# Optimization experiments

Hardware: AMD Instinct MI355X
Metric: run time of the kernel (lower is better)

## Reference

```python
import jax, jax.numpy as jnp
import numpy as np

N = 8192
F_IN = 690
F_OUT = 690
H = 3
ALPHA = 0.2  # LeakyReLU negative slope
NEG_INF = -9e15


def setup_inputs() -> dict:
    key = jax.random.key(0)
    k1, k2, k3, k4 = jax.random.split(key, 4)
    x = jax.random.normal(k1, (N, F_IN), dtype=jnp.float32)
    adj = jax.random.randint(k2, (N, N), 0, 2, dtype=jnp.int32)
    adj = adj.at[jnp.arange(N), jnp.arange(N)].set(1)  # self-loops, as in eye() init
    # Xavier-ish scaled params, stacked over heads
    W = jax.random.normal(k3, (H, F_IN, F_OUT), dtype=jnp.float32) * 0.05
    a = jax.random.normal(k4, (H, 2 * F_OUT, 1), dtype=jnp.float32) * 0.05
    return {"x": x, "adj": adj, "W": W, "a": a}


def reference(x, adj, W, a):
    # Wh per head: [H, N, F_OUT]
    Wh = jnp.einsum('nf,hfo->hno', x, W)
    # Additive decomposition of concat-based score: e_ij = leakyrelu(a1_i + a2_j)
    a1 = jnp.einsum('hno,ho->hn', Wh, a[:, :F_OUT, 0])  # [H, N]
    a2 = jnp.einsum('hno,ho->hn', Wh, a[:, F_OUT:, 0])  # [H, N]
    e = jax.nn.leaky_relu(a1[:, :, None] + a2[:, None, :], negative_slope=ALPHA)  # [H, N, N]
    e = jnp.where(adj[None, :, :] > 0, e, NEG_INF)
    attn = jax.nn.softmax(e, axis=-1)
    h_prime = jnp.einsum('hnm,hmo->hno', attn, Wh)  # [H, N, F_OUT]
    # GAT(concat=False): mean over heads, then ELU (dropout is identity in eval)
    y = jax.nn.elu(jnp.mean(h_prime, axis=0))  # [N, F_OUT]
    return y
```

## Files before the change

kernel.cpp:

```cpp
#include <hip/hip_runtime.h>
#include <hip/hip_bf16.h>
#include <stdint.h>

#define NN 8192
#define FD 690
#define NH 3
#define KPAD 704
#define OPAD 768
#define USTRIDE 704
#define KS 2
#define LOG2E 1.4426950408889634f

typedef __attribute__((ext_vector_type(8))) short bf16x8;
typedef __attribute__((ext_vector_type(4))) float f32x4;

typedef __attribute__((address_space(1))) const void gas_t;
typedef __attribute__((address_space(3))) void las_t;

__device__ __forceinline__ void async_ld16(const void* g, void* l) {
  __builtin_amdgcn_global_load_lds((gas_t*)g, (las_t*)l, 16, 0, 0);
}

__device__ __forceinline__ float bf2f(unsigned short u) {
  return __uint_as_float(((unsigned int)u) << 16);
}
__device__ __forceinline__ unsigned short f2bf(float f) {
  __hip_bfloat16 h = __float2bfloat16(f);
  return *reinterpret_cast<unsigned short*>(&h);
}
__device__ __forceinline__ float selbit(float e, uint32_t lo, uint32_t hi) {
  uint64_t m = ((uint64_t)hi << 32) | lo;
  float r;
  asm("v_cndmask_b32 %0, 0, %1, %2" : "=v"(r) : "v"(e), "s"(m));
  return r;
}

__global__ __launch_bounds__(256) void k_cast(const float* __restrict__ x,
                                              const float* __restrict__ W,
                                              unsigned short* __restrict__ xb,
                                              unsigned short* __restrict__ wt) {
  int q = blockIdx.x * 256 + threadIdx.x;
  const int XQ = NN * KPAD / 4;
  if (q < XQ) {
    int idx = q * 4;
    int n = idx / KPAD, f = idx - n * KPAD;
    uint2 out;
    if (f + 3 < FD) {
      const float* xp = &x[(size_t)n * FD + f];
      float2 a = *reinterpret_cast<const float2*>(xp);
      float2 b = *reinterpret_cast<const float2*>(xp + 2);
      out.x = (uint32_t)f2bf(a.x) | ((uint32_t)f2bf(a.y) << 16);
      out.y = (uint32_t)f2bf(b.x) | ((uint32_t)f2bf(b.y) << 16);
    } else {
      unsigned short e[4];
#pragma unroll
      for (int t = 0; t < 4; ++t) {
        int ff = f + t;
        e[t] = (ff < FD) ? f2bf(x[(size_t)n * FD + ff]) : 0;
      }
      out.x = (uint32_t)e[0] | ((uint32_t)e[1] << 16);
      out.y = (uint32_t)e[2] | ((uint32_t)e[3] << 16);
    }
    *reinterpret_cast<uint2*>(&xb[idx]) = out;
    return;
  }
  int idx = q - XQ;
  if (idx >= NH * OPAD * KPAD) return;
  int h = idx / (OPAD * KPAD);
  int rem = idx - h * OPAD * KPAD;
  int o = rem / KPAD, f = rem - o * KPAD;
  float v = (o < FD && f < FD) ? W[((size_t)h * FD + f) * FD + o] : 0.f;
  wt[idx] = f2bf(v);
}

__global__ __launch_bounds__(256) void k_pack(const int4* __restrict__ adj4,
                                              uint64_t* __restrict__ bm) {
  int gw = (blockIdx.x * 256 + threadIdx.x) >> 6;
  int lane = threadIdx.x & 63;
  int i = gw >> 5, seg = gw & 31;
  int4 v = adj4[(size_t)i * (NN / 4) + seg * 64 + lane];
  uint32_t nib = (uint32_t)(v.x > 0) | ((uint32_t)(v.y > 0) << 1)
               | ((uint32_t)(v.z > 0) << 2) | ((uint32_t)(v.w > 0) << 3);
  nib |= __shfl_xor(nib, 1) << 4;
  nib |= __shfl_xor(nib, 2) << 8;
  nib |= __shfl_xor(nib, 4) << 16;
  uint32_t hi = __shfl_xor(nib, 8);
  if ((lane & 15) == 0)
    bm[(size_t)i * 128 + seg * 4 + (lane >> 4)] = (uint64_t)nib | ((uint64_t)hi << 32);
}

__global__ __launch_bounds__(512) void k_gemm_wht(const unsigned short* __restrict__ wt,
                                                  const unsigned short* __restrict__ xb,
                                                  const float* __restrict__ a,
                                                  unsigned short* __restrict__ wht,
                                                  float* __restrict__ a1acc,
                                                  float* __restrict__ a2acc) {
  const int m0 = blockIdx.x * 128;
  const int n0 = blockIdx.y * 256;
  const int h  = blockIdx.z;
  const int tid = threadIdx.x;
  const int w = tid >> 6, l = tid & 63;
  const int wm = w >> 2, wn = w & 3;
  __shared__ unsigned short As[128 * 64];
  __shared__ unsigned short Bs[256 * 64];
  const unsigned short* Ag = wt + (size_t)h * OPAD * KPAD;
  f32x4 acc[4][4] = {};
  for (int kt = 0; kt < KPAD / 64; ++kt) {
    const int k0 = kt * 64;
#pragma unroll
    for (int r = 0; r < 2; ++r) {
      const unsigned short* g = Ag + (size_t)(m0 + r * 64 + w * 8 + (l >> 3)) * KPAD + k0 + (l & 7) * 8;
      async_ld16(g, &As[(r * 64 + w * 8) * 64]);
    }
#pragma unroll
    for (int r = 0; r < 4; ++r) {
      const unsigned short* g = xb + (size_t)(n0 + r * 64 + w * 8 + (l >> 3)) * KPAD + k0 + (l & 7) * 8;
      async_ld16(g, &Bs[(r * 64 + w * 8) * 64]);
    }
    __syncthreads();
#pragma unroll
    for (int ks = 0; ks < 2; ++ks) {
      bf16x8 af[4], bfr[4];
#pragma unroll
      for (int mi = 0; mi < 4; ++mi)
        af[mi] = *reinterpret_cast<const bf16x8*>(
            &As[(wm * 64 + mi * 16 + (l & 15)) * 64 + ks * 32 + (l >> 4) * 8]);
#pragma unroll
      for (int ni = 0; ni < 4; ++ni)
        bfr[ni] = *reinterpret_cast<const bf16x8*>(
            &Bs[(wn * 64 + ni * 16 + (l & 15)) * 64 + ks * 32 + (l >> 4) * 8]);
#pragma unroll
      for (int mi = 0; mi < 4; ++mi)
#pragma unroll
        for (int ni = 0; ni < 4; ++ni)
          acc[mi][ni] = __builtin_amdgcn_mfma_f32_16x16x32_bf16(af[mi], bfr[ni], acc[mi][ni], 0, 0, 0);
    }
    __syncthreads();
  }
  unsigned short* Wh = wht + (size_t)h * OPAD * NN;
#pragma unroll
  for (int mi = 0; mi < 4; ++mi)
#pragma unroll
    for (int j = 0; j < 4; ++j) {
      int o = m0 + wm * 64 + mi * 16 + (l >> 4) * 4 + j;
#pragma unroll
      for (int ni = 0; ni < 4; ++ni) {
        int n = n0 + wn * 64 + ni * 16 + (l & 15);
        float val = (o == FD) ? 1.0f : acc[mi][ni][j];
        Wh[(size_t)o * NN + n] = f2bf(val);
      }
    }
  const float* ap1 = a + h * 2 * FD;
  const float* ap2 = ap1 + FD;
  float av1[4][4], av2[4][4];
#pragma unroll
  for (int mi = 0; mi < 4; ++mi)
#pragma unroll
    for (int j = 0; j < 4; ++j) {
      int o = m0 + wm * 64 + mi * 16 + (l >> 4) * 4 + j;
      bool ok = (o < FD);
      av1[mi][j] = ok ? ap1[o] : 0.f;
      av2[mi][j] = ok ? ap2[o] : 0.f;
    }
#pragma unroll
  for (int ni = 0; ni < 4; ++ni) {
    float p1 = 0.f, p2 = 0.f;
#pragma unroll
    for (int mi = 0; mi < 4; ++mi)
#pragma unroll
      for (int j = 0; j < 4; ++j) {
        p1 += acc[mi][ni][j] * av1[mi][j];
        p2 += acc[mi][ni][j] * av2[mi][j];
      }
    int n = n0 + wn * 64 + ni * 16 + (l & 15);
    unsafeAtomicAdd(&a1acc[h * NN + n], p1);
    unsafeAtomicAdd(&a2acc[h * NN + n], p2);
  }
}

__global__ __launch_bounds__(256) void k_exp(const float* __restrict__ a1acc,
                                             const float* __restrict__ a2acc,
                                             float* __restrict__ e1s, float* __restrict__ f1s,
                                             float* __restrict__ e2s, float* __restrict__ f2s) {
  int i = blockIdx.x * 256 + threadIdx.x;
  if (i >= NH * NN) return;
  float s1 = a1acc[i] * LOG2E, s2 = a2acc[i] * LOG2E;
  e1s[i] = exp2f(s1);
  f1s[i] = exp2f(0.2f * s1);
  e2s[i] = exp2f(s2);
  f2s[i] = exp2f(0.2f * s2);
}

__global__ __launch_bounds__(512, 4) void k_pv(const unsigned short* __restrict__ wht,
                                               const float* __restrict__ e1s,
                                               const float* __restrict__ f1s,
                                               const float* __restrict__ e2s,
                                               const float* __restrict__ f2s,
                                               const uint64_t* __restrict__ bm,
                                               float* __restrict__ U0,
                                               float* __restrict__ U1,
                                               int plain) {
  const int m0 = blockIdx.x * 64;
  const int n0 = blockIdx.y * 384;
  const int h    = blockIdx.z / KS;
  const int kseg = blockIdx.z % KS;
  const int tid = threadIdx.x;
  const int w = tid >> 6, l = tid & 63;
  const int wu = __builtin_amdgcn_readfirstlane(w);
  __shared__ unsigned short As[64 * 64];
  __shared__ unsigned short Bs[384 * 64];
  const unsigned short* Bg = wht + (size_t)h * OPAD * NN;
  const uint64_t* bmw = bm + (size_t)(m0 + wu * 8) * 128;
  float E1v[8], F1v[8];
#pragma unroll
  for (int r = 0; r < 8; ++r) {
    E1v[r] = e1s[h * NN + m0 + wu * 8 + r];
    F1v[r] = f1s[h * NN + m0 + wu * 8 + r];
  }

  const int kt0 = kseg * (NN / 64 / KS);
  const int ktend = kt0 + NN / 64 / KS;

  f32x4 acc[4][3] = {};

  for (int kt = kt0; kt < ktend; ++kt) {
    const int k0 = kt * 64;
    const float e2v = e2s[h * NN + k0 + l];
    const float f2v = f2s[h * NN + k0 + l];
#pragma unroll
    for (int call = 0; call < 6; ++call) {
      int c = call * 512 + tid;
      int row = c >> 3;
      int kb  = c & 7;
      int kbs = kb ^ (row & 7);
      const unsigned short* g = Bg + (size_t)(n0 + row) * NN + k0 + kbs * 8;
      async_ld16(g, &Bs[(size_t)c * 8]);
    }
#pragma unroll
    for (int r = 0; r < 8; ++r) {
      uint64_t mrow = bmw[(size_t)r * 128 + kt];
      uint32_t mlo = __builtin_amdgcn_readfirstlane((uint32_t)mrow);
      uint32_t mhi = __builtin_amdgcn_readfirstlane((uint32_t)(mrow >> 32));
      float e = fmaxf(E1v[r] * e2v, F1v[r] * f2v);
      e = selbit(e, mlo, mhi);
      As[(wu * 8 + r) * 64 + (l ^ (r << 3))] = f2bf(e);
    }
    __syncthreads();

#pragma unroll
    for (int ks = 0; ks < 2; ++ks) {
      bf16x8 af[4], bfr[3];
#pragma unroll
      for (int mi = 0; mi < 4; ++mi) {
        int row = mi * 16 + (l & 15);
        af[mi] = *reinterpret_cast<const bf16x8*>(
            &As[row * 64 + (((ks * 4 + (l >> 4)) ^ (row & 7)) * 8)]);
      }
#pragma unroll
      for (int ni = 0; ni < 3; ++ni) {
        int row = w * 48 + ni * 16 + (l & 15);
        bfr[ni] = *reinterpret_cast<const bf16x8*>(
            &Bs[row * 64 + (((ks * 4 + (l >> 4)) ^ (row & 7)) * 8)]);
      }
#pragma unroll
      for (int mi = 0; mi < 4; ++mi)
#pragma unroll
        for (int ni = 0; ni < 3; ++ni)
          acc[mi][ni] = __builtin_amdgcn_mfma_f32_16x16x32_bf16(af[mi], bfr[ni], acc[mi][ni], 0, 0, 0);
    }
    __syncthreads();
  }

  float* Ud = (kseg == 0) ? U0 : U1;
#pragma unroll
  for (int mi = 0; mi < 4; ++mi)
#pragma unroll
    for (int j = 0; j < 4; ++j) {
      int i = m0 + mi * 16 + (l >> 4) * 4 + j;
#pragma unroll
      for (int ni = 0; ni < 3; ++ni) {
        int n = n0 + w * 48 + ni * 16 + (l & 15);
        if (n <= FD) {
          size_t off = ((size_t)h * NN + i) * USTRIDE + n;
          if (plain) Ud[off] = acc[mi][ni][j];
          else       unsafeAtomicAdd(&U0[off], acc[mi][ni][j]);
        }
      }
    }
}

__global__ __launch_bounds__(256) void k_final(const float* __restrict__ U0,
                                               const float* __restrict__ U1,
                                               float* __restrict__ y,
                                               int two) {
  int idx = blockIdx.x * 256 + threadIdx.x;
  if (idx >= NN * (FD / 2)) return;
  int i = idx / (FD / 2), p = idx - i * (FD / 2);
  int o = p * 2;
  const size_t HS = (size_t)NN * USTRIDE;
  float s0 = 0.f, s1 = 0.f;
#pragma unroll
  for (int h = 0; h < NH; ++h) {
    size_t b = h * HS + (size_t)i * USTRIDE;
    float2 u = *reinterpret_cast<const float2*>(&U0[b + o]);
    float z = U0[b + FD];
    if (two) {
      float2 u2 = *reinterpret_cast<const float2*>(&U1[b + o]);
      u.x += u2.x; u.y += u2.y;
      z += U1[b + FD];
    }
    float zi = 1.0f / z;
    s0 += u.x * zi;
    s1 += u.y * zi;
  }
  s0 *= (1.f / 3.f);
  s1 *= (1.f / 3.f);
  float2 out;
  out.x = s0 > 0.f ? s0 : (expf(s0) - 1.f);
  out.y = s1 > 0.f ? s1 : (expf(s1) - 1.f);
  *reinterpret_cast<float2*>(&y[(size_t)i * FD + o]) = out;
}

extern "C" void kernel_launch(void* const* d_in, const int* in_sizes, int n_in,
                              void* d_out, int out_size, void* d_ws, size_t ws_size,
                              hipStream_t stream) {
  const float* x   = (const float*)d_in[0];
  const int*   adj = (const int*)d_in[1];
  const float* W   = (const float*)d_in[2];
  const float* a   = (const float*)d_in[3];
  float* y = (float*)d_out;

  char* ws = (char*)d_ws;
  size_t off = 0;
  auto alloc = [&](size_t bytes) {
    void* p = ws + off;
    off = (off + bytes + 255) & ~(size_t)255;
    return p;
  };
  unsigned short* xb  = (unsigned short*)alloc((size_t)NN * KPAD * 2);
  unsigned short* wt  = (unsigned short*)alloc((size_t)NH * OPAD * KPAD * 2);
  unsigned short* wht = (unsigned short*)alloc((size_t)NH * OPAD * NN * 2);
  float* e1s = (float*)alloc((size_t)NH * NN * 4);
  float* f1s = (float*)alloc((size_t)NH * NN * 4);
  float* e2s = (float*)alloc((size_t)NH * NN * 4);
  float* f2s = (float*)alloc((size_t)NH * NN * 4);
  uint64_t* bm = (uint64_t*)alloc((size_t)NN * 128 * 8);
  float* U0 = (float*)alloc((size_t)NH * NN * USTRIDE * 4);
  float* a1acc = (float*)alloc((size_t)NH * NN * 4);
  float* a2acc = (float*)alloc((size_t)NH * NN * 4);
  const size_t usize = (size_t)NH * NN * USTRIDE * 4;
  bool two = (ws_size >= off + usize + 256);
  float* U1 = two ? (float*)alloc(usize) : U0;
  (void)in_sizes; (void)n_in; (void)out_size;

  if (!two) hipMemsetAsync(U0, 0, usize, stream);
  hipMemsetAsync(a1acc, 0, (size_t)NH * NN * 4 * 2, stream);

  const int cast_total = NN * KPAD / 4 + NH * OPAD * KPAD;
  k_cast<<<(cast_total + 255) / 256, 256, 0, stream>>>(x, W, xb, wt);
  k_pack<<<NN * 32 * 64 / 256, 256, 0, stream>>>((const int4*)adj, bm);
  k_gemm_wht<<<dim3(OPAD / 128, NN / 256, NH), 512, 0, stream>>>(wt, xb, a, wht, a1acc, a2acc);
  k_exp<<<(NH * NN + 255) / 256, 256, 0, stream>>>(a1acc, a2acc, e1s, f1s, e2s, f2s);
  k_pv<<<dim3(NN / 64, 2, NH * KS), 512, 0, stream>>>(wht, e1s, f1s, e2s, f2s, bm,
                                                      U0, U1, two ? 1 : 0);
  k_final<<<(NN * (FD / 2) + 255) / 256, 256, 0, stream>>>(U0, U1, y, two ? 1 : 0);
}
```

Baseline: 547.5 us.

## Fuse adjacency bit-packing into GEMM launch and fold accumulator zeroing into cast

Runs the adjacency bitmask packing in extra blocks of the same grid as the Wh GEMM, so the memory-bound adj read overlaps with the compute-bound GEMM. Zeroing of the a1/a2 accumulators moves from a memset into the cast kernel, removing a separate launch. The cost is a larger, heterogeneous kernel whose pack blocks share the GEMM's LDS allocation and 512-thread launch bounds, which may limit occupancy.

```diff
diff --git a/kernel.cpp b/kernel.cpp
--- a/kernel.cpp
+++ b/kernel.cpp
@@ -9,6 +9,8 @@
 #define OPAD 768
 #define USTRIDE 704
 #define KS 2
+#define GW_BLOCKS 576
+#define PK_BLOCKS 1024
 #define LOG2E 1.4426950408889634f
 
 typedef __attribute__((ext_vector_type(8))) short bf16x8;
@@ -38,7 +40,8 @@
 __global__ __launch_bounds__(256) void k_cast(const float* __restrict__ x,
                                               const float* __restrict__ W,
                                               unsigned short* __restrict__ xb,
-                                              unsigned short* __restrict__ wt) {
+                                              unsigned short* __restrict__ wt,
+                                              float4* __restrict__ accz) {
   int q = blockIdx.x * 256 + threadIdx.x;
   const int XQ = NN * KPAD / 4;
   if (q < XQ) {
@@ -65,44 +68,56 @@
     return;
   }
   int idx = q - XQ;
-  if (idx >= NH * OPAD * KPAD) return;
-  int h = idx / (OPAD * KPAD);
-  int rem = idx - h * OPAD * KPAD;
-  int o = rem / KPAD, f = rem - o * KPAD;
-  float v = (o < FD && f < FD) ? W[((size_t)h * FD + f) * FD + o] : 0.f;
-  wt[idx] = f2bf(v);
-}
-
-__global__ __launch_bounds__(256) void k_pack(const int4* __restrict__ adj4,
-                                              uint64_t* __restrict__ bm) {
-  int gw = (blockIdx.x * 256 + threadIdx.x) >> 6;
-  int lane = threadIdx.x & 63;
-  int i = gw >> 5, seg = gw & 31;
-  int4 v = adj4[(size_t)i * (NN / 4) + seg * 64 + lane];
-  uint32_t nib = (uint32_t)(v.x > 0) | ((uint32_t)(v.y > 0) << 1)
-               | ((uint32_t)(v.z > 0) << 2) | ((uint32_t)(v.w > 0) << 3);
-  nib |= __shfl_xor(nib, 1) << 4;
-  nib |= __shfl_xor(nib, 2) << 8;
-  nib |= __shfl_xor(nib, 4) << 16;
-  uint32_t hi = __shfl_xor(nib, 8);
-  if ((lane & 15) == 0)
-    bm[(size_t)i * 128 + seg * 4 + (lane >> 4)] = (uint64_t)nib | ((uint64_t)hi << 32);
-}
-
-__global__ __launch_bounds__(512) void k_gemm_wht(const unsigned short* __restrict__ wt,
-                                                  const unsigned short* __restrict__ xb,
-                                                  const float* __restrict__ a,
-                                                  unsigned short* __restrict__ wht,
-                                                  float* __restrict__ a1acc,
-                                                  float* __restrict__ a2acc) {
-  const int m0 = blockIdx.x * 128;
-  const int n0 = blockIdx.y * 256;
-  const int h  = blockIdx.z;
+  if (idx < NH * OPAD * KPAD) {
+    int h = idx / (OPAD * KPAD);
+    int rem = idx - h * OPAD * KPAD;
+    int o = rem / KPAD, f = rem - o * KPAD;
+    float v = (o < FD && f < FD) ? W[((size_t)h * FD + f) * FD + o] : 0.f;
+    wt[idx] = f2bf(v);
+    return;
+  }
+  idx -= NH * OPAD * KPAD;
+  if (idx < 2 * NH * NN / 4) {
+    float4 z; z.x = 0.f; z.y = 0.f; z.z = 0.f; z.w = 0.f;
+    accz[idx] = z;
+  }
+}
+
+__global__ __launch_bounds__(512) void k_gw_pack(const unsigned short* __restrict__ wt,
+                                                 const unsigned short* __restrict__ xb,
+                                                 const float* __restrict__ a,
+                                                 unsigned short* __restrict__ wht,
+                                                 float* __restrict__ a1acc,
+                                                 float* __restrict__ a2acc,
+                                                 const int4* __restrict__ adj4,
+                                                 uint64_t* __restrict__ bm) {
+  __shared__ unsigned short As[128 * 64];
+  __shared__ unsigned short Bs[256 * 64];
   const int tid = threadIdx.x;
+  if (blockIdx.x >= GW_BLOCKS) {
+    const int pid = blockIdx.x - GW_BLOCKS;
+    const int lane = tid & 63;
+    int task = pid * 8 + (tid >> 6);
+    for (int t = 0; t < 32; ++t, task += PK_BLOCKS * 8) {
+      int i = task >> 5, seg = task & 31;
+      int4 v = adj4[(size_t)i * (NN / 4) + seg * 64 + lane];
+      uint32_t nib = (uint32_t)(v.x > 0) | ((uint32_t)(v.y > 0) << 1)
+                   | ((uint32_t)(v.z > 0) << 2) | ((uint32_t)(v.w > 0) << 3);
+      nib |= __shfl_xor(nib, 1) << 4;
+      nib |= __shfl_xor(nib, 2) << 8;
+      nib |= __shfl_xor(nib, 4) << 16;
+      uint32_t hi = __shfl_xor(nib, 8);
+      if ((lane & 15) == 0)
+        bm[(size_t)i * 128 + seg * 4 + (lane >> 4)] = (uint64_t)nib | ((uint64_t)hi << 32);
+    }
+    return;
+  }
+  const int bx = blockIdx.x;
+  const int m0 = (bx % 6) * 128;
+  const int n0 = ((bx / 6) % 32) * 256;
+  const int h  = bx / 192;
   const int w = tid >> 6, l = tid & 63;
   const int wm = w >> 2, wn = w & 3;
-  __shared__ unsigned short As[128 * 64];
-  __shared__ unsigned short Bs[256 * 64];
   const unsigned short* Ag = wt + (size_t)h * OPAD * KPAD;
   f32x4 acc[4][4] = {};
   for (int kt = 0; kt < KPAD / 64; ++kt) {
@@ -354,12 +369,11 @@
   (void)in_sizes; (void)n_in; (void)out_size;
 
   if (!two) hipMemsetAsync(U0, 0, usize, stream);
-  hipMemsetAsync(a1acc, 0, (size_t)NH * NN * 4 * 2, stream);
-
-  const int cast_total = NN * KPAD / 4 + NH * OPAD * KPAD;
-  k_cast<<<(cast_total + 255) / 256, 256, 0, stream>>>(x, W, xb, wt);
-  k_pack<<<NN * 32 * 64 / 256, 256, 0, stream>>>((const int4*)adj, bm);
-  k_gemm_wht<<<dim3(OPAD / 128, NN / 256, NH), 512, 0, stream>>>(wt, xb, a, wht, a1acc, a2acc);
+
+  const int cast_total = NN * KPAD / 4 + NH * OPAD * KPAD + 2 * NH * NN / 4;
+  k_cast<<<(cast_total + 255) / 256, 256, 0, stream>>>(x, W, xb, wt, (float4*)a1acc);
+  k_gw_pack<<<GW_BLOCKS + PK_BLOCKS, 512, 0, stream>>>(wt, xb, a, wht, a1acc, a2acc,
+                                                       (const int4*)adj, bm);
   k_exp<<<(NH * NN + 255) / 256, 256, 0, stream>>>(a1acc, a2acc, e1s, f1s, e2s, f2s);
   k_pv<<<dim3(NN / 64, 2, NH * KS), 512, 0, stream>>>(wht, e1s, f1s, e2s, f2s, bm,
                                                       U0, U1, two ? 1 : 0);
```

After: 555.7 us. About the same (+1.5%).
